# Performance work log

Hardware: AMD Instinct MI355X
Metric: run time of the kernel (lower is better)

Reference implementation:

```python
import jax, jax.numpy as jnp
import numpy as np

N = 50000   # nodes
E = 800000  # directed edges (built as reverse pairs so rev mapping is exact)
F = 64      # node_feat_dim
FE = 64     # edge_feat_dim
M = 64      # message_dim
S = 3       # num_status
L = 4       # number_layers

def _lin(key, din, dout):
    w = jax.random.normal(key, (din, dout), jnp.float32) * np.float32(1.0 / np.sqrt(din))
    return w, jnp.zeros((dout,), jnp.float32)

def setup_inputs() -> dict:
    key = jax.random.key(0)
    ks = jax.random.split(key, 16)
    half = E // 2
    s = jax.random.randint(ks[0], (half,), 0, N)
    t = jax.random.randint(ks[1], (half,), 0, N)
    src = jnp.concatenate([s, t])                      # source node of each edge
    tgt = jnp.concatenate([t, s])                      # target node of each edge
    rev = jnp.concatenate([jnp.arange(half, E), jnp.arange(half)])  # reverse-edge index
    inp = dict(src=src, tgt=tgt, rev=rev)
    inp['edge_feat_raw'] = jax.random.uniform(ks[2], (E, 1), jnp.float32)
    inp['node_prob'] = jax.random.uniform(ks[3], (N, 1), jnp.float32)
    inp['node_seed'] = (jax.random.uniform(ks[4], (N, 1)) < 0.05).astype(jnp.float32)
    inp['W_node'], inp['b_node'] = _lin(ks[5], 2, F)
    inp['W_edge'], inp['b_edge'] = _lin(ks[6], 1, FE)
    inp['W_init'], inp['b_init'] = _lin(ks[7], F + FE, M)
    inp['W_aggr'], inp['b_aggr'] = _lin(ks[8], M, M)
    inp['W_out'], inp['b_out'] = _lin(ks[9], M + F, S)
    inp['W_me'], inp['b_me'] = _lin(ks[10], FE + M, M)
    inp['W_mp'], inp['b_mp'] = _lin(ks[11], M, M)
    inp['W_ih'] = jax.random.normal(ks[12], (3 * M, M), jnp.float32) * np.float32(1.0 / np.sqrt(M))
    inp['W_hh'] = jax.random.normal(ks[13], (3 * M, M), jnp.float32) * np.float32(1.0 / np.sqrt(M))
    inp['b_ih'] = jnp.zeros((3 * M,), jnp.float32)
    inp['b_hh'] = jnp.zeros((3 * M,), jnp.float32)
    return inp

def reference(src, tgt, rev, edge_feat_raw, node_prob, node_seed,
              W_node, b_node, W_edge, b_edge, W_init, b_init,
              W_aggr, b_aggr, W_out, b_out, W_me, b_me, W_mp, b_mp,
              W_ih, W_hh, b_ih, b_hh):
    relu = jax.nn.relu
    node_feat = relu(jnp.concatenate([node_prob, node_seed], 1) @ W_node + b_node)  # [N,F]
    snode_feat = node_feat[src]                                                      # snode2edge gather [E,F]
    edge_feat = relu(edge_feat_raw @ W_edge + b_edge)                                # [E,FE]
    message = relu(jnp.concatenate([snode_feat, edge_feat], 1) @ W_init + b_init)    # [E,M]

    def nodes_out(msg):
        agg = jax.ops.segment_sum(msg, tgt, num_segments=N)                          # edge2tnode scatter-add
        agg = relu(agg @ W_aggr + b_aggr)
        logits = relu(jnp.concatenate([agg, node_feat], 1) @ W_out + b_out)
        return jax.nn.log_softmax(logits, axis=1)                                    # [N,S]

    def gru(x, h):  # torch.nn.GRUCell semantics
        gi = x @ W_ih.T + b_ih
        gh = h @ W_hh.T + b_hh
        ir, iz, in_ = jnp.split(gi, 3, axis=1)
        hr, hz, hn = jnp.split(gh, 3, axis=1)
        r = jax.nn.sigmoid(ir + hr)
        z = jax.nn.sigmoid(iz + hz)
        n = jnp.tanh(in_ + r * hn)
        return (1.0 - z) * n + z * h

    marg = [nodes_out(message)]
    deltas = []
    for _ in range(L):
        m = relu(jnp.concatenate([message, edge_feat], 1) @ W_me + b_me)
        node_agg = jax.ops.segment_sum(m, tgt, num_segments=N)
        m = node_agg[src] - m[rev]                                                   # nb_matrix (non-backtracking) spmm
        m = relu(m @ W_mp + b_mp)
        message = gru(m, message)
        marg.append(nodes_out(message))
        deltas.append(jnp.max(jnp.abs(jnp.exp(marg[-2][:, -1]) - jnp.exp(marg[-1][:, -1]))))
    return jnp.stack(marg, 0), jnp.stack(deltas)
```

## Files before the change

kernel.cpp:

```cpp
#include <hip/hip_runtime.h>
#include <hip/hip_fp16.h>

typedef _Float16 half8 __attribute__((ext_vector_type(8)));
typedef float floatx4 __attribute__((ext_vector_type(4)));

#define DEV static __device__ __forceinline__

DEV float sigmoidf_(float x) { return 1.f / (1.f + __expf(-x)); }
DEV float tanh_fast(float x) {
    x = fminf(fmaxf(x, -15.f), 15.f);
    float e2 = __expf(2.f * x);
    return (e2 - 1.f) / (e2 + 1.f);
}
DEV unsigned short f2h_(float f) {
    __half h = __float2half_rn(f);
    return *reinterpret_cast<unsigned short*>(&h);
}
DEV float h2f_(unsigned short u) {
    __half h = *reinterpret_cast<__half*>(&u);
    return __half2float(h);
}
DEV float loadElem(const float* p) { return *p; }
DEV float loadElem(const unsigned short* p) { return h2f_(*p); }
DEV void storeMsg(float* p, float v) { *p = v; }
DEV void storeMsg(unsigned short* p, float v) { *p = f2h_(v); }

DEV half8 afrag(const float* __restrict__ p, unsigned off) {
    float4 a = *reinterpret_cast<const float4*>(p + off);
    float4 b = *reinterpret_cast<const float4*>(p + off + 4);
    half8 h;
    h[0] = (_Float16)a.x; h[1] = (_Float16)a.y; h[2] = (_Float16)a.z; h[3] = (_Float16)a.w;
    h[4] = (_Float16)b.x; h[5] = (_Float16)b.y; h[6] = (_Float16)b.z; h[7] = (_Float16)b.w;
    return h;
}
DEV half8 afrag(const unsigned short* __restrict__ p, unsigned off) {
    uint4 v = *reinterpret_cast<const uint4*>(p + off);
    return __builtin_bit_cast(half8, v);
}
DEV half8 h8load(const _Float16* __restrict__ p) {
    return *reinterpret_cast<const half8*>(p);
}
DEV half8 effrag(float er, const float* __restrict__ We,
                 const float* __restrict__ be, int k0) {
    float4 w0 = *reinterpret_cast<const float4*>(We + k0);
    float4 w1 = *reinterpret_cast<const float4*>(We + k0 + 4);
    float4 b0 = *reinterpret_cast<const float4*>(be + k0);
    float4 b1 = *reinterpret_cast<const float4*>(be + k0 + 4);
    half8 h;
    h[0] = (_Float16)fmaxf(fmaf(er, w0.x, b0.x), 0.f);
    h[1] = (_Float16)fmaxf(fmaf(er, w0.y, b0.y), 0.f);
    h[2] = (_Float16)fmaxf(fmaf(er, w0.z, b0.z), 0.f);
    h[3] = (_Float16)fmaxf(fmaf(er, w0.w, b0.w), 0.f);
    h[4] = (_Float16)fmaxf(fmaf(er, w1.x, b1.x), 0.f);
    h[5] = (_Float16)fmaxf(fmaf(er, w1.y, b1.y), 0.f);
    h[6] = (_Float16)fmaxf(fmaf(er, w1.z, b1.z), 0.f);
    h[7] = (_Float16)fmaxf(fmaf(er, w1.w, b1.w), 0.f);
    return h;
}
DEV void load8(const float* __restrict__ p, float x[8]) {
    const float4* q = reinterpret_cast<const float4*>(p);
    float4 a = q[0], b = q[1];
    x[0] = a.x; x[1] = a.y; x[2] = a.z; x[3] = a.w;
    x[4] = b.x; x[5] = b.y; x[6] = b.z; x[7] = b.w;
}

__global__ void k_deg(const int* __restrict__ tgt, int* __restrict__ deg, int E) {
    int e = blockIdx.x * blockDim.x + threadIdx.x;
    if (e < E) atomicAdd(&deg[tgt[e]], 1);
}

__global__ __launch_bounds__(1024)
void k_scan(const int* __restrict__ deg, int* __restrict__ row_ptr,
            int* __restrict__ cursor, int N) {
    __shared__ int part[1024];
    int tid = threadIdx.x;
    int chunk = (N + 1023) / 1024;
    int lo = tid * chunk, hi = min(lo + chunk, N);
    int s = 0;
    for (int i = lo; i < hi; i++) s += deg[i];
    part[tid] = s;
    __syncthreads();
    for (int off = 1; off < 1024; off <<= 1) {
        int v = (tid >= off) ? part[tid - off] : 0;
        __syncthreads();
        part[tid] += v;
        __syncthreads();
    }
    int base = (tid == 0) ? 0 : part[tid - 1];
    for (int i = lo; i < hi; i++) {
        row_ptr[i] = base;
        cursor[i] = base;
        base += deg[i];
    }
    if (tid == 1023) row_ptr[N] = part[1023];
}

__global__ void k_fill(const int* __restrict__ tgt, int* __restrict__ cursor,
                       int* __restrict__ col_idx, int E) {
    int e = blockIdx.x * blockDim.x + threadIdx.x;
    if (e < E) {
        int pos = atomicAdd(&cursor[tgt[e]], 1);
        col_idx[pos] = e;
    }
}

__global__ void k_prep(const float* __restrict__ Wme, const float* __restrict__ Wmp,
                       const float* __restrict__ Wi, const float* __restrict__ Wih,
                       const float* __restrict__ Whh, _Float16* __restrict__ wp) {
    int t = blockIdx.x * blockDim.x + threadIdx.x;
    if (t < 8192) { int n = t >> 7, k = t & 127; wp[t] = (_Float16)Wme[k * 64 + n]; return; }
    int u = t - 8192;
    if (u < 4096) { int n = u >> 6, k = u & 63; wp[8192 + u] = (_Float16)Wmp[k * 64 + n]; return; }
    u -= 4096;
    if (u < 4096) { int n = u >> 6, k = u & 63; wp[12288 + u] = (_Float16)Wi[(64 + k) * 64 + n]; return; }
    u -= 4096;
    if (u < 12288) { wp[16384 + u] = (_Float16)Wih[u]; return; }
    u -= 12288;
    if (u < 12288) { wp[28672 + u] = (_Float16)Whh[u]; return; }
}

__global__ __launch_bounds__(256)
void k_zn(const float* __restrict__ prob, const float* __restrict__ seedp,
          const float* __restrict__ Wn, const float* __restrict__ bn,
          const float* __restrict__ Wi, const float* __restrict__ bi,
          float* __restrict__ zn, int N) {
    int n = blockIdx.x * blockDim.x + threadIdx.x;
    if (n >= N) return;
    float p = prob[n], sd = seedp[n];
    float acc[64];
#pragma unroll
    for (int j = 0; j < 64; j++) acc[j] = bi[j];
#pragma unroll 1
    for (int k = 0; k < 64; k++) {
        float nf = fmaxf(fmaf(p, Wn[k], fmaf(sd, Wn[64 + k], bn[k])), 0.f);
        const float* w = Wi + k * 64;
#pragma unroll
        for (int j = 0; j < 64; j++) acc[j] = fmaf(nf, w[j], acc[j]);
    }
    float4* q = reinterpret_cast<float4*>(zn + (size_t)n * 64);
#pragma unroll
    for (int c = 0; c < 16; c++)
        q[c] = make_float4(acc[4 * c], acc[4 * c + 1], acc[4 * c + 2], acc[4 * c + 3]);
}

template <typename MsgT, bool FULL>
__global__ __launch_bounds__(256)
void k_init_mfma(const int* __restrict__ src, const float* __restrict__ eraw,
                 const float* __restrict__ We, const float* __restrict__ be,
                 const _Float16* __restrict__ WibT, const float* __restrict__ zn,
                 MsgT* __restrict__ message, int row_off, int E) {
    int wid = (blockIdx.x * blockDim.x + threadIdx.x) >> 6;
    int rowbase = row_off + wid * 64;
    if (rowbase >= E) return;
    int lane = threadIdx.x & 63, q = lane >> 4, m16 = lane & 15, kq8 = q * 8;
    floatx4 zero4 = {0.f, 0.f, 0.f, 0.f};
    floatx4 acc[4][4];
#pragma unroll
    for (int a = 0; a < 4; a++)
#pragma unroll
        for (int b = 0; b < 4; b++) acc[a][b] = zero4;
#pragma unroll
    for (int ks = 0; ks < 2; ks++) {
        int k0 = ks * 32 + kq8;
        half8 B[4];
#pragma unroll
        for (int nt = 0; nt < 4; nt++) B[nt] = h8load(WibT + (nt * 16 + m16) * 64 + k0);
#pragma unroll
        for (int rt = 0; rt < 4; rt++) {
            int row = rowbase + rt * 16 + m16;
            if (!FULL) row = min(row, E - 1);
            half8 A = effrag(eraw[row], We, be, k0);
#pragma unroll
            for (int nt = 0; nt < 4; nt++)
                acc[rt][nt] = __builtin_amdgcn_mfma_f32_16x16x32_f16(A, B[nt], acc[rt][nt], 0, 0, 0);
        }
    }
#pragma unroll
    for (int nt = 0; nt < 4; nt++) {
        int col = nt * 16 + m16;
#pragma unroll
        for (int rt = 0; rt < 4; rt++)
#pragma unroll
            for (int r = 0; r < 4; r++) {
                int row = rowbase + rt * 16 + q * 4 + r;
                if (FULL || row < E) {
                    int s = src[row];
                    float v = acc[rt][nt][r] + zn[(unsigned)s * 64u + col];
                    storeMsg(message + (unsigned)row * 64u + col, fmaxf(v, 0.f));
                }
            }
    }
}

template <typename MsgT, bool FULL>
__global__ __launch_bounds__(256)
void k_edge_m_mfma(const float* __restrict__ eraw, const float* __restrict__ We,
                   const float* __restrict__ be, const _Float16* __restrict__ WmeT,
                   const float* __restrict__ bme, const MsgT* __restrict__ message,
                   unsigned short* __restrict__ m_buf, int row_off, int E) {
    int wid = (blockIdx.x * blockDim.x + threadIdx.x) >> 6;
    int rowbase = row_off + wid * 64;
    if (rowbase >= E) return;
    int lane = threadIdx.x & 63, q = lane >> 4, m16 = lane & 15, kq8 = q * 8;
    floatx4 zero4 = {0.f, 0.f, 0.f, 0.f};
    floatx4 acc[4][4];
#pragma unroll
    for (int a = 0; a < 4; a++)
#pragma unroll
        for (int b = 0; b < 4; b++) acc[a][b] = zero4;
#pragma unroll
    for (int ks = 0; ks < 4; ks++) {
        int k0 = ks * 32 + kq8;
        half8 B[4];
#pragma unroll
        for (int nt = 0; nt < 4; nt++) B[nt] = h8load(WmeT + (nt * 16 + m16) * 128 + k0);
#pragma unroll
        for (int rt = 0; rt < 4; rt++) {
            int row = rowbase + rt * 16 + m16;
            if (!FULL) row = min(row, E - 1);
            half8 A = (ks < 2) ? afrag(message + (unsigned)row * 64u, k0)
                               : effrag(eraw[row], We, be, k0 - 64);
#pragma unroll
            for (int nt = 0; nt < 4; nt++)
                acc[rt][nt] = __builtin_amdgcn_mfma_f32_16x16x32_f16(A, B[nt], acc[rt][nt], 0, 0, 0);
        }
    }
#pragma unroll
    for (int nt = 0; nt < 4; nt++) {
        int col = nt * 16 + m16;
        float bb = bme[col];
#pragma unroll
        for (int rt = 0; rt < 4; rt++)
#pragma unroll
            for (int r = 0; r < 4; r++) {
                int row = rowbase + rt * 16 + q * 4 + r;
                if (FULL || row < E)
                    m_buf[(unsigned)row * 64u + col] = f2h_(fmaxf(acc[rt][nt][r] + bb, 0.f));
            }
    }
}

template <typename MsgT, bool FULL>
__global__ __launch_bounds__(256)
void k_gru_mfma(const int* __restrict__ src, const int* __restrict__ rev,
                const float* __restrict__ node_agg,
                const unsigned short* __restrict__ m_buf,
                const _Float16* __restrict__ WmpT, const float* __restrict__ bmp,
                const _Float16* __restrict__ WihP, const _Float16* __restrict__ WhhP,
                const float* __restrict__ bih, const float* __restrict__ bhh,
                MsgT* __restrict__ message, int row_off, int E) {
    __shared__ _Float16 uT[4][64 * 72];
    int wid = (blockIdx.x * blockDim.x + threadIdx.x) >> 6;
    int rowbase = row_off + wid * 64;
    if (rowbase >= E) return;
    int w = threadIdx.x >> 6;
    int lane = threadIdx.x & 63, q = lane >> 4, m16 = lane & 15, kq8 = q * 8;
    floatx4 zero4 = {0.f, 0.f, 0.f, 0.f};

    floatx4 accU[4][4];
#pragma unroll
    for (int a = 0; a < 4; a++)
#pragma unroll
        for (int b = 0; b < 4; b++) accU[a][b] = zero4;
#pragma unroll
    for (int ks = 0; ks < 2; ks++) {
        int k0 = ks * 32 + kq8;
        half8 B[4];
#pragma unroll
        for (int nt = 0; nt < 4; nt++) B[nt] = h8load(WmpT + (nt * 16 + m16) * 64 + k0);
#pragma unroll
        for (int rt = 0; rt < 4; rt++) {
            int row = rowbase + rt * 16 + m16;
            if (!FULL) row = min(row, E - 1);
            int s = src[row], rv = rev[row];
            const float* na = node_agg + (unsigned)s * 64u + k0;
            float4 a0 = *reinterpret_cast<const float4*>(na);
            float4 a1 = *reinterpret_cast<const float4*>(na + 4);
            uint4 mv = *reinterpret_cast<const uint4*>(m_buf + (unsigned)rv * 64u + k0);
            half8 mh = __builtin_bit_cast(half8, mv);
            half8 A;
            A[0] = (_Float16)(a0.x - (float)mh[0]); A[1] = (_Float16)(a0.y - (float)mh[1]);
            A[2] = (_Float16)(a0.z - (float)mh[2]); A[3] = (_Float16)(a0.w - (float)mh[3]);
            A[4] = (_Float16)(a1.x - (float)mh[4]); A[5] = (_Float16)(a1.y - (float)mh[5]);
            A[6] = (_Float16)(a1.z - (float)mh[6]); A[7] = (_Float16)(a1.w - (float)mh[7]);
#pragma unroll
            for (int nt = 0; nt < 4; nt++)
                accU[rt][nt] = __builtin_amdgcn_mfma_f32_16x16x32_f16(A, B[nt], accU[rt][nt], 0, 0, 0);
        }
    }
#pragma unroll
    for (int nt = 0; nt < 4; nt++) {
        int col = nt * 16 + m16;
        float bb = bmp[col];
#pragma unroll
        for (int rt = 0; rt < 4; rt++)
#pragma unroll
            for (int r = 0; r < 4; r++) {
                int rl = rt * 16 + q * 4 + r;
                uT[w][rl * 72 + col] = (_Float16)fmaxf(accU[rt][nt][r] + bb, 0.f);
            }
    }
    half8 au[4][2], ah[4][2];
#pragma unroll
    for (int rt = 0; rt < 4; rt++)
#pragma unroll
        for (int ks = 0; ks < 2; ks++) {
            au[rt][ks] = *reinterpret_cast<const half8*>(
                &uT[w][(rt * 16 + m16) * 72 + ks * 32 + kq8]);
            int row = rowbase + rt * 16 + m16;
            if (!FULL) row = min(row, E - 1);
            ah[rt][ks] = afrag(message + (unsigned)row * 64u, ks * 32 + kq8);
        }
#pragma unroll 1
    for (int nt = 0; nt < 4; nt++) {
        int col = nt * 16 + m16;
        half8 Bir[2], Biz[2], Bin[2], Bhr[2], Bhz[2], Bhn[2];
#pragma unroll
        for (int ks = 0; ks < 2; ks++) {
            int k0 = ks * 32 + kq8;
            Bir[ks] = h8load(WihP + (unsigned)(0 + col) * 64u + k0);
            Biz[ks] = h8load(WihP + (unsigned)(64 + col) * 64u + k0);
            Bin[ks] = h8load(WihP + (unsigned)(128 + col) * 64u + k0);
            Bhr[ks] = h8load(WhhP + (unsigned)(0 + col) * 64u + k0);
            Bhz[ks] = h8load(WhhP + (unsigned)(64 + col) * 64u + k0);
            Bhn[ks] = h8load(WhhP + (unsigned)(128 + col) * 64u + k0);
        }
        floatx4 ar[4], az[4], ain[4], ahn[4];
#pragma unroll
        for (int rt = 0; rt < 4; rt++) { ar[rt] = zero4; az[rt] = zero4; ain[rt] = zero4; ahn[rt] = zero4; }
#pragma unroll
        for (int ks = 0; ks < 2; ks++)
#pragma unroll
            for (int rt = 0; rt < 4; rt++) {
                ar[rt] = __builtin_amdgcn_mfma_f32_16x16x32_f16(au[rt][ks], Bir[ks], ar[rt], 0, 0, 0);
                ar[rt] = __builtin_amdgcn_mfma_f32_16x16x32_f16(ah[rt][ks], Bhr[ks], ar[rt], 0, 0, 0);
                az[rt] = __builtin_amdgcn_mfma_f32_16x16x32_f16(au[rt][ks], Biz[ks], az[rt], 0, 0, 0);
                az[rt] = __builtin_amdgcn_mfma_f32_16x16x32_f16(ah[rt][ks], Bhz[ks], az[rt], 0, 0, 0);
                ain[rt] = __builtin_amdgcn_mfma_f32_16x16x32_f16(au[rt][ks], Bin[ks], ain[rt], 0, 0, 0);
                ahn[rt] = __builtin_amdgcn_mfma_f32_16x16x32_f16(ah[rt][ks], Bhn[ks], ahn[rt], 0, 0, 0);
            }
        float br_ = bih[col] + bhh[col];
        float bz_ = bih[64 + col] + bhh[64 + col];
        float bin_ = bih[128 + col];
        float bhn_ = bhh[128 + col];
#pragma unroll
        for (int rt = 0; rt < 4; rt++)
#pragma unroll
            for (int r = 0; r < 4; r++) {
                int row = rowbase + rt * 16 + q * 4 + r;
                if (FULL || row < E) {
                    float rr = sigmoidf_(ar[rt][r] + br_);
                    float zz = sigmoidf_(az[rt][r] + bz_);
                    float nn = tanh_fast(ain[rt][r] + bin_ + rr * (ahn[rt][r] + bhn_));
                    MsgT* mp = message + (unsigned)row * 64u + col;
                    float hv = loadElem(mp);
                    storeMsg(mp, fmaf(zz, hv - nn, nn));
                }
            }
    }
}

template <typename T>
__global__ __launch_bounds__(256)
void k_agg(const int* __restrict__ row_ptr, const int* __restrict__ col_idx,
           const T* __restrict__ rows, float* __restrict__ out, int N) {
    int wid = (blockIdx.x * blockDim.x + threadIdx.x) >> 6;
    int lane = threadIdx.x & 63;
    if (wid >= N) return;
    int beg = row_ptr[wid], end = row_ptr[wid + 1];
    float acc = 0.f;
    int i = beg;
    for (; i + 3 < end; i += 4) {
        int e0 = __builtin_amdgcn_readfirstlane(col_idx[i]);
        int e1 = __builtin_amdgcn_readfirstlane(col_idx[i + 1]);
        int e2 = __builtin_amdgcn_readfirstlane(col_idx[i + 2]);
        int e3 = __builtin_amdgcn_readfirstlane(col_idx[i + 3]);
        acc += loadElem(rows + (unsigned)e0 * 64u + lane);
        acc += loadElem(rows + (unsigned)e1 * 64u + lane);
        acc += loadElem(rows + (unsigned)e2 * 64u + lane);
        acc += loadElem(rows + (unsigned)e3 * 64u + lane);
    }
    for (; i < end; i++) {
        int e0 = __builtin_amdgcn_readfirstlane(col_idx[i]);
        acc += loadElem(rows + (unsigned)e0 * 64u + lane);
    }
    out[(unsigned)wid * 64u + lane] = acc;
}

__global__ __launch_bounds__(256, 2)
void k_nodes(const float* __restrict__ node_agg, const float* __restrict__ prob,
             const float* __restrict__ seedp,
             const float* __restrict__ Wn, const float* __restrict__ bn,
             const float* __restrict__ Wa, const float* __restrict__ ba,
             const float* __restrict__ Wo, const float* __restrict__ bo,
             float* __restrict__ marg, float* __restrict__ prev_p2,
             float* __restrict__ deltas_f, int layer, int N) {
    int n = blockIdx.x * blockDim.x + threadIdx.x;
    if (n >= N) return;
    float a[64];
#pragma unroll
    for (int j = 0; j < 64; j++) a[j] = ba[j];
    const float* ag = node_agg + (size_t)n * 64;
#pragma unroll 1
    for (int c = 0; c < 8; c++) {
        float v[8];
        load8(ag + 8 * c, v);
#pragma unroll
        for (int i = 0; i < 8; i++) {
            const float* w = Wa + (8 * c + i) * 64;
#pragma unroll
            for (int j = 0; j < 64; j++) a[j] = fmaf(v[i], w[j], a[j]);
        }
    }
    float l0 = bo[0], l1 = bo[1], l2 = bo[2];
#pragma unroll
    for (int k = 0; k < 64; k++) {
        float ak = fmaxf(a[k], 0.f);
        l0 = fmaf(ak, Wo[k * 3 + 0], l0);
        l1 = fmaf(ak, Wo[k * 3 + 1], l1);
        l2 = fmaf(ak, Wo[k * 3 + 2], l2);
    }
    float p = prob[n], sd = seedp[n];
#pragma unroll 1
    for (int k = 0; k < 64; k++) {
        float nf = fmaxf(fmaf(p, Wn[k], fmaf(sd, Wn[64 + k], bn[k])), 0.f);
        l0 = fmaf(nf, Wo[(64 + k) * 3 + 0], l0);
        l1 = fmaf(nf, Wo[(64 + k) * 3 + 1], l1);
        l2 = fmaf(nf, Wo[(64 + k) * 3 + 2], l2);
    }
    l0 = fmaxf(l0, 0.f); l1 = fmaxf(l1, 0.f); l2 = fmaxf(l2, 0.f);
    float mx = fmaxf(l0, fmaxf(l1, l2));
    float ssum = __expf(l0 - mx) + __expf(l1 - mx) + __expf(l2 - mx);
    float lse = mx + logf(ssum);
    float o0 = l0 - lse, o1 = l1 - lse, o2 = l2 - lse;
    float* out = marg + ((size_t)layer * N + n) * 3;
    out[0] = o0; out[1] = o1; out[2] = o2;
    float p2 = __expf(o2);
    if (layer > 0) {
        float d = fabsf(p2 - prev_p2[n]);
        atomicMax(reinterpret_cast<unsigned int*>(deltas_f + (layer - 1)),
                  __float_as_uint(d));
    }
    prev_p2[n] = p2;
}

__global__ void k_deltas_out(const float* __restrict__ deltas_f,
                             float* __restrict__ out, int L) {
    int i = threadIdx.x;
    if (i < L) out[i] = deltas_f[i];
}

template <typename MsgT>
static void run_pipeline(void* const* d_in, int E, int N, MsgT* message,
                         unsigned short* m_buf, float* node_agg, _Float16* wp,
                         int* deg, int* row_ptr, int* cursor, int* col_idx,
                         float* prev_p2, float* deltas_f, float* marg,
                         float* deltas_out, hipStream_t stream) {
    const int* src = (const int*)d_in[0];
    const int* tgt = (const int*)d_in[1];
    const int* rev = (const int*)d_in[2];
    const float* eraw = (const float*)d_in[3];
    const float* prob = (const float*)d_in[4];
    const float* seedp = (const float*)d_in[5];
    const float* Wn = (const float*)d_in[6];  const float* bn = (const float*)d_in[7];
    const float* We = (const float*)d_in[8];  const float* be = (const float*)d_in[9];
    const float* Wi = (const float*)d_in[10]; const float* bi = (const float*)d_in[11];
    const float* Wa = (const float*)d_in[12]; const float* ba = (const float*)d_in[13];
    const float* Wo = (const float*)d_in[14]; const float* bo = (const float*)d_in[15];
    const float* Wme = (const float*)d_in[16]; const float* bme = (const float*)d_in[17];
    const float* Wmp = (const float*)d_in[18]; const float* bmp = (const float*)d_in[19];
    const float* Wih = (const float*)d_in[20]; const float* Whh = (const float*)d_in[21];
    const float* bih = (const float*)d_in[22]; const float* bhh = (const float*)d_in[23];

    const _Float16* WmeT = wp;
    const _Float16* WmpT = wp + 8192;
    const _Float16* WibT = wp + 12288;
    const _Float16* WihP = wp + 16384;
    const _Float16* WhhP = wp + 28672;

    const int L = 4;
    dim3 blk(256);
    dim3 eg((E + 255) / 256), ng((N + 255) / 256);
    dim3 ag((N + 3) / 4);
    int fullb = E / 256;
    int tail_off = fullb * 256;
    bool tail = (tail_off < E);

    hipMemsetAsync(deg, 0, (size_t)N * 4, stream);
    hipMemsetAsync(deltas_f, 0, L * sizeof(float), stream);
    k_deg<<<eg, blk, 0, stream>>>(tgt, deg, E);
    k_scan<<<1, 1024, 0, stream>>>(deg, row_ptr, cursor, N);
    k_fill<<<eg, blk, 0, stream>>>(tgt, cursor, col_idx, E);
    k_prep<<<160, 256, 0, stream>>>(Wme, Wmp, Wi, Wih, Whh, wp);
    k_zn<<<ng, blk, 0, stream>>>(prob, seedp, Wn, bn, Wi, bi, node_agg, N);

    if (fullb)
        k_init_mfma<MsgT, true><<<fullb, blk, 0, stream>>>(src, eraw, We, be, WibT,
                                                           node_agg, message, 0, E);
    if (tail)
        k_init_mfma<MsgT, false><<<1, blk, 0, stream>>>(src, eraw, We, be, WibT,
                                                        node_agg, message, tail_off, E);
    k_agg<MsgT><<<ag, blk, 0, stream>>>(row_ptr, col_idx, message, node_agg, N);
    k_nodes<<<ng, blk, 0, stream>>>(node_agg, prob, seedp, Wn, bn, Wa, ba, Wo, bo,
                                    marg, prev_p2, deltas_f, 0, N);
    for (int l = 0; l < L; l++) {
        if (fullb)
            k_edge_m_mfma<MsgT, true><<<fullb, blk, 0, stream>>>(eraw, We, be, WmeT, bme,
                                                                 message, m_buf, 0, E);
        if (tail)
            k_edge_m_mfma<MsgT, false><<<1, blk, 0, stream>>>(eraw, We, be, WmeT, bme,
                                                              message, m_buf, tail_off, E);
        k_agg<unsigned short><<<ag, blk, 0, stream>>>(row_ptr, col_idx, m_buf,
                                                      node_agg, N);
        if (fullb)
            k_gru_mfma<MsgT, true><<<fullb, blk, 0, stream>>>(src, rev, node_agg, m_buf,
                                                              WmpT, bmp, WihP, WhhP,
                                                              bih, bhh, message, 0, E);
        if (tail)
            k_gru_mfma<MsgT, false><<<1, blk, 0, stream>>>(src, rev, node_agg, m_buf,
                                                           WmpT, bmp, WihP, WhhP,
                                                           bih, bhh, message, tail_off, E);
        k_agg<MsgT><<<ag, blk, 0, stream>>>(row_ptr, col_idx, message, node_agg, N);
        k_nodes<<<ng, blk, 0, stream>>>(node_agg, prob, seedp, Wn, bn, Wa, ba,
                                        Wo, bo, marg, prev_p2, deltas_f, l + 1, N);
    }
    k_deltas_out<<<1, 64, 0, stream>>>(deltas_f, deltas_out, L);
}

extern "C" void kernel_launch(void* const* d_in, const int* in_sizes, int n_in,
                              void* d_out, int out_size, void* d_ws, size_t ws_size,
                              hipStream_t stream) {
    const int E = in_sizes[0];
    const int N = in_sizes[4];
    const int L = 4, S = 3;

    float* marg = (float*)d_out;
    float* deltas_out = marg + (size_t)(L + 1) * N * S;

    char* ws = (char*)d_ws;
    float* deltas_f = (float*)ws;
    float* prev_p2 = (float*)(ws + 16);
    int* deg = (int*)(prev_p2 + N);
    int* row_ptr = deg + N;
    int* cursor = row_ptr + N + 1;
    int* col_idx = cursor + N;
    char* p = (char*)(col_idx + E);
    p = (char*)(((uintptr_t)p + 255) & ~(uintptr_t)255);
    _Float16* wp = (_Float16*)p;
    p += 40960 * 2;
    p = (char*)(((uintptr_t)p + 255) & ~(uintptr_t)255);
    float* node_agg = (float*)p;
    p += (size_t)N * 64 * 4;
    p = (char*)(((uintptr_t)p + 255) & ~(uintptr_t)255);
    size_t head = (size_t)(p - ws);
    size_t msg_f32 = (size_t)E * 64 * 4;
    size_t msg_f16 = (size_t)E * 64 * 2;
    size_t m_f16 = (size_t)E * 64 * 2;

    if (ws_size >= head + msg_f32 + m_f16) {
        float* message = (float*)p;
        unsigned short* m_buf = (unsigned short*)(p + msg_f32);
        run_pipeline<float>(d_in, E, N, message, m_buf, node_agg, wp,
                            deg, row_ptr, cursor, col_idx,
                            prev_p2, deltas_f, marg, deltas_out, stream);
    } else {
        unsigned short* message = (unsigned short*)p;
        unsigned short* m_buf = (unsigned short*)(p + msg_f16);
        run_pipeline<unsigned short>(d_in, E, N, message, m_buf, node_agg, wp,
                                     deg, row_ptr, cursor, col_idx,
                                     prev_p2, deltas_f, marg, deltas_out, stream);
    }
}
```

Measured before the change: 1.998 ms.

## Process 16-row subtiles sequentially in edge MFMA kernels and widen aggregation unroll

The init, edge-message and GRU MFMA kernels now walk each wave's 64 rows one 16-row subtile at a time in a non-unrolled loop, instead of holding a 4x4 accumulator grid and all A fragments at once. This shrinks accumulator and fragment register use, and the GRU's shared-memory staging buffer drops from 64 to 16 rows per wave, with the aim of raising occupancy. In exchange, weight B fragments are reloaded for every subtile rather than reused across four row tiles. The aggregation kernel is unrolled to 8 gathered rows per iteration with two accumulators, to keep more loads in flight.

New measurement: 2.659 ms. 1.33x slower.

```diff
diff --git a/kernel.cpp b/kernel.cpp
--- a/kernel.cpp
+++ b/kernel.cpp
@@ -154,41 +154,37 @@
     if (rowbase >= E) return;
     int lane = threadIdx.x & 63, q = lane >> 4, m16 = lane & 15, kq8 = q * 8;
     floatx4 zero4 = {0.f, 0.f, 0.f, 0.f};
-    floatx4 acc[4][4];
-#pragma unroll
-    for (int a = 0; a < 4; a++)
-#pragma unroll
-        for (int b = 0; b < 4; b++) acc[a][b] = zero4;
-#pragma unroll
-    for (int ks = 0; ks < 2; ks++) {
-        int k0 = ks * 32 + kq8;
-        half8 B[4];
-#pragma unroll
-        for (int nt = 0; nt < 4; nt++) B[nt] = h8load(WibT + (nt * 16 + m16) * 64 + k0);
-#pragma unroll
-        for (int rt = 0; rt < 4; rt++) {
-            int row = rowbase + rt * 16 + m16;
-            if (!FULL) row = min(row, E - 1);
-            half8 A = effrag(eraw[row], We, be, k0);
-#pragma unroll
-            for (int nt = 0; nt < 4; nt++)
-                acc[rt][nt] = __builtin_amdgcn_mfma_f32_16x16x32_f16(A, B[nt], acc[rt][nt], 0, 0, 0);
-        }
-    }
-#pragma unroll
-    for (int nt = 0; nt < 4; nt++) {
-        int col = nt * 16 + m16;
-#pragma unroll
-        for (int rt = 0; rt < 4; rt++)
+#pragma unroll 1
+    for (int rt = 0; rt < 4; rt++) {
+        int rbase = rowbase + rt * 16;
+        int row = rbase + m16;
+        if (!FULL) row = min(row, E - 1);
+        float er = eraw[row];
+        half8 A0 = effrag(er, We, be, kq8);
+        half8 A1 = effrag(er, We, be, 32 + kq8);
+        floatx4 acc[4];
+#pragma unroll
+        for (int nt = 0; nt < 4; nt++) acc[nt] = zero4;
+#pragma unroll
+        for (int nt = 0; nt < 4; nt++) {
+            half8 B0 = h8load(WibT + (nt * 16 + m16) * 64 + kq8);
+            half8 B1 = h8load(WibT + (nt * 16 + m16) * 64 + 32 + kq8);
+            acc[nt] = __builtin_amdgcn_mfma_f32_16x16x32_f16(A0, B0, acc[nt], 0, 0, 0);
+            acc[nt] = __builtin_amdgcn_mfma_f32_16x16x32_f16(A1, B1, acc[nt], 0, 0, 0);
+        }
+#pragma unroll
+        for (int nt = 0; nt < 4; nt++) {
+            int col = nt * 16 + m16;
 #pragma unroll
             for (int r = 0; r < 4; r++) {
-                int row = rowbase + rt * 16 + q * 4 + r;
-                if (FULL || row < E) {
-                    int s = src[row];
-                    float v = acc[rt][nt][r] + zn[(unsigned)s * 64u + col];
-                    storeMsg(message + (unsigned)row * 64u + col, fmaxf(v, 0.f));
+                int orow = rbase + q * 4 + r;
+                if (FULL || orow < E) {
+                    int s = src[orow];
+                    float v = acc[nt][r] + zn[(unsigned)s * 64u + col];
+                    storeMsg(message + (unsigned)orow * 64u + col, fmaxf(v, 0.f));
                 }
             }
+        }
     }
 }
 
@@ -203,40 +199,39 @@
     if (rowbase >= E) return;
     int lane = threadIdx.x & 63, q = lane >> 4, m16 = lane & 15, kq8 = q * 8;
     floatx4 zero4 = {0.f, 0.f, 0.f, 0.f};
-    floatx4 acc[4][4];
-#pragma unroll
-    for (int a = 0; a < 4; a++)
-#pragma unroll
-        for (int b = 0; b < 4; b++) acc[a][b] = zero4;
-#pragma unroll
-    for (int ks = 0; ks < 4; ks++) {
-        int k0 = ks * 32 + kq8;
-        half8 B[4];
-#pragma unroll
-        for (int nt = 0; nt < 4; nt++) B[nt] = h8load(WmeT + (nt * 16 + m16) * 128 + k0);
-#pragma unroll
-        for (int rt = 0; rt < 4; rt++) {
-            int row = rowbase + rt * 16 + m16;
-            if (!FULL) row = min(row, E - 1);
-            half8 A = (ks < 2) ? afrag(message + (unsigned)row * 64u, k0)
-                               : effrag(eraw[row], We, be, k0 - 64);
-#pragma unroll
-            for (int nt = 0; nt < 4; nt++)
-                acc[rt][nt] = __builtin_amdgcn_mfma_f32_16x16x32_f16(A, B[nt], acc[rt][nt], 0, 0, 0);
-        }
-    }
-#pragma unroll
-    for (int nt = 0; nt < 4; nt++) {
-        int col = nt * 16 + m16;
-        float bb = bme[col];
-#pragma unroll
-        for (int rt = 0; rt < 4; rt++)
+#pragma unroll 1
+    for (int rt = 0; rt < 4; rt++) {
+        int rbase = rowbase + rt * 16;
+        int row = rbase + m16;
+        if (!FULL) row = min(row, E - 1);
+        float er = eraw[row];
+        half8 A[4];
+        A[0] = afrag(message + (unsigned)row * 64u, kq8);
+        A[1] = afrag(message + (unsigned)row * 64u, 32 + kq8);
+        A[2] = effrag(er, We, be, kq8);
+        A[3] = effrag(er, We, be, 32 + kq8);
+        floatx4 acc[4];
+#pragma unroll
+        for (int nt = 0; nt < 4; nt++) acc[nt] = zero4;
+#pragma unroll
+        for (int ks = 0; ks < 4; ks++) {
+#pragma unroll
+            for (int nt = 0; nt < 4; nt++) {
+                half8 B = h8load(WmeT + (nt * 16 + m16) * 128 + ks * 32 + kq8);
+                acc[nt] = __builtin_amdgcn_mfma_f32_16x16x32_f16(A[ks], B, acc[nt], 0, 0, 0);
+            }
+        }
+#pragma unroll
+        for (int nt = 0; nt < 4; nt++) {
+            int col = nt * 16 + m16;
+            float bb = bme[col];
 #pragma unroll
             for (int r = 0; r < 4; r++) {
-                int row = rowbase + rt * 16 + q * 4 + r;
-                if (FULL || row < E)
-                    m_buf[(unsigned)row * 64u + col] = f2h_(fmaxf(acc[rt][nt][r] + bb, 0.f));
+                int orow = rbase + q * 4 + r;
+                if (FULL || orow < E)
+                    m_buf[(unsigned)orow * 64u + col] = f2h_(fmaxf(acc[nt][r] + bb, 0.f));
             }
+        }
     }
 }
 
@@ -249,7 +244,7 @@
                 const _Float16* __restrict__ WihP, const _Float16* __restrict__ WhhP,
                 const float* __restrict__ bih, const float* __restrict__ bhh,
                 MsgT* __restrict__ message, int row_off, int E) {
-    __shared__ _Float16 uT[4][64 * 72];
+    __shared__ _Float16 uT[4][16 * 72];
     int wid = (blockIdx.x * blockDim.x + threadIdx.x) >> 6;
     int rowbase = row_off + wid * 64;
     if (rowbase >= E) return;
@@ -257,22 +252,21 @@
     int lane = threadIdx.x & 63, q = lane >> 4, m16 = lane & 15, kq8 = q * 8;
     floatx4 zero4 = {0.f, 0.f, 0.f, 0.f};
 
-    floatx4 accU[4][4];
-#pragma unroll
-    for (int a = 0; a < 4; a++)
-#pragma unroll
-        for (int b = 0; b < 4; b++) accU[a][b] = zero4;
-#pragma unroll
-    for (int ks = 0; ks < 2; ks++) {
-        int k0 = ks * 32 + kq8;
-        half8 B[4];
-#pragma unroll
-        for (int nt = 0; nt < 4; nt++) B[nt] = h8load(WmpT + (nt * 16 + m16) * 64 + k0);
-#pragma unroll
-        for (int rt = 0; rt < 4; rt++) {
-            int row = rowbase + rt * 16 + m16;
-            if (!FULL) row = min(row, E - 1);
-            int s = src[row], rv = rev[row];
+#pragma unroll 1
+    for (int rt = 0; rt < 4; rt++) {
+        int rbase = rowbase + rt * 16;
+        int row = rbase + m16;
+        if (!FULL) row = min(row, E - 1);
+        int s = src[row], rv = rev[row];
+        half8 ah0 = afrag(message + (unsigned)row * 64u, kq8);
+        half8 ah1 = afrag(message + (unsigned)row * 64u, 32 + kq8);
+
+        floatx4 accU[4];
+#pragma unroll
+        for (int nt = 0; nt < 4; nt++) accU[nt] = zero4;
+#pragma unroll
+        for (int ks = 0; ks < 2; ks++) {
+            int k0 = ks * 32 + kq8;
             const float* na = node_agg + (unsigned)s * 64u + k0;
             float4 a0 = *reinterpret_cast<const float4*>(na);
             float4 a1 = *reinterpret_cast<const float4*>(na + 4);
@@ -284,79 +278,61 @@
             A[4] = (_Float16)(a1.x - (float)mh[4]); A[5] = (_Float16)(a1.y - (float)mh[5]);
             A[6] = (_Float16)(a1.z - (float)mh[6]); A[7] = (_Float16)(a1.w - (float)mh[7]);
 #pragma unroll
-            for (int nt = 0; nt < 4; nt++)
-                accU[rt][nt] = __builtin_amdgcn_mfma_f32_16x16x32_f16(A, B[nt], accU[rt][nt], 0, 0, 0);
-        }
-    }
-#pragma unroll
-    for (int nt = 0; nt < 4; nt++) {
-        int col = nt * 16 + m16;
-        float bb = bmp[col];
-#pragma unroll
-        for (int rt = 0; rt < 4; rt++)
+            for (int nt = 0; nt < 4; nt++) {
+                half8 B = h8load(WmpT + (nt * 16 + m16) * 64 + k0);
+                accU[nt] = __builtin_amdgcn_mfma_f32_16x16x32_f16(A, B, accU[nt], 0, 0, 0);
+            }
+        }
+#pragma unroll
+        for (int nt = 0; nt < 4; nt++) {
+            int col = nt * 16 + m16;
+            float bb = bmp[col];
+#pragma unroll
+            for (int r = 0; r < 4; r++)
+                uT[w][(q * 4 + r) * 72 + col] = (_Float16)fmaxf(accU[nt][r] + bb, 0.f);
+        }
+        half8 au0 = *reinterpret_cast<const half8*>(&uT[w][m16 * 72 + kq8]);
+        half8 au1 = *reinterpret_cast<const half8*>(&uT[w][m16 * 72 + 32 + kq8]);
+
+#pragma unroll 1
+        for (int nt = 0; nt < 4; nt++) {
+            int col = nt * 16 + m16;
+            floatx4 ar = zero4, az = zero4, ain = zero4, ahn = zero4;
+#pragma unroll
+            for (int ks = 0; ks < 2; ks++) {
+                int k0 = ks * 32 + kq8;
+                half8 au = ks ? au1 : au0;
+                half8 ah = ks ? ah1 : ah0;
+                half8 Bir = h8load(WihP + (unsigned)(0 + col) * 64u + k0);
+                half8 Biz = h8load(WihP + (unsigned)(64 + col) * 64u + k0);
+                half8 Bin = h8load(WihP + (unsigned)(128 + col) * 64u + k0);
+                half8 Bhr = h8load(WhhP + (unsigned)(0 + col) * 64u + k0);
+                half8 Bhz = h8load(WhhP + (unsigned)(64 + col) * 64u + k0);
+                half8 Bhn = h8load(WhhP + (unsigned)(128 + col) * 64u + k0);
+                ar = __builtin_amdgcn_mfma_f32_16x16x32_f16(au, Bir, ar, 0, 0, 0);
+                ar = __builtin_amdgcn_mfma_f32_16x16x32_f16(ah, Bhr, ar, 0, 0, 0);
+                az = __builtin_amdgcn_mfma_f32_16x16x32_f16(au, Biz, az, 0, 0, 0);
+                az = __builtin_amdgcn_mfma_f32_16x16x32_f16(ah, Bhz, az, 0, 0, 0);
+                ain = __builtin_amdgcn_mfma_f32_16x16x32_f16(au, Bin, ain, 0, 0, 0);
+                ahn = __builtin_amdgcn_mfma_f32_16x16x32_f16(ah, Bhn, ahn, 0, 0, 0);
+            }
+            float br_ = bih[col] + bhh[col];
+            float bz_ = bih[64 + col] + bhh[64 + col];
+            float bin_ = bih[128 + col];
+            float bhn_ = bhh[128 + col];
 #pragma unroll
             for (int r = 0; r < 4; r++) {
-                int rl = rt * 16 + q * 4 + r;
-                uT[w][rl * 72 + col] = (_Float16)fmaxf(accU[rt][nt][r] + bb, 0.f);
-            }
-    }
-    half8 au[4][2], ah[4][2];
-#pragma unroll
-    for (int rt = 0; rt < 4; rt++)
-#pragma unroll
-        for (int ks = 0; ks < 2; ks++) {
-            au[rt][ks] = *reinterpret_cast<const half8*>(
-                &uT[w][(rt * 16 + m16) * 72 + ks * 32 + kq8]);
-            int row = rowbase + rt * 16 + m16;
-            if (!FULL) row = min(row, E - 1);
-            ah[rt][ks] = afrag(message + (unsigned)row * 64u, ks * 32 + kq8);
-        }
-#pragma unroll 1
-    for (int nt = 0; nt < 4; nt++) {
-        int col = nt * 16 + m16;
-        half8 Bir[2], Biz[2], Bin[2], Bhr[2], Bhz[2], Bhn[2];
-#pragma unroll
-        for (int ks = 0; ks < 2; ks++) {
-            int k0 = ks * 32 + kq8;
-            Bir[ks] = h8load(WihP + (unsigned)(0 + col) * 64u + k0);
-            Biz[ks] = h8load(WihP + (unsigned)(64 + col) * 64u + k0);
-            Bin[ks] = h8load(WihP + (unsigned)(128 + col) * 64u + k0);
-            Bhr[ks] = h8load(WhhP + (unsigned)(0 + col) * 64u + k0);
-            Bhz[ks] = h8load(WhhP + (unsigned)(64 + col) * 64u + k0);
-            Bhn[ks] = h8load(WhhP + (unsigned)(128 + col) * 64u + k0);
-        }
-        floatx4 ar[4], az[4], ain[4], ahn[4];
-#pragma unroll
-        for (int rt = 0; rt < 4; rt++) { ar[rt] = zero4; az[rt] = zero4; ain[rt] = zero4; ahn[rt] = zero4; }
-#pragma unroll
-        for (int ks = 0; ks < 2; ks++)
-#pragma unroll
-            for (int rt = 0; rt < 4; rt++) {
-                ar[rt] = __builtin_amdgcn_mfma_f32_16x16x32_f16(au[rt][ks], Bir[ks], ar[rt], 0, 0, 0);
-                ar[rt] = __builtin_amdgcn_mfma_f32_16x16x32_f16(ah[rt][ks], Bhr[ks], ar[rt], 0, 0, 0);
-                az[rt] = __builtin_amdgcn_mfma_f32_16x16x32_f16(au[rt][ks], Biz[ks], az[rt], 0, 0, 0);
-                az[rt] = __builtin_amdgcn_mfma_f32_16x16x32_f16(ah[rt][ks], Bhz[ks], az[rt], 0, 0, 0);
-                ain[rt] = __builtin_amdgcn_mfma_f32_16x16x32_f16(au[rt][ks], Bin[ks], ain[rt], 0, 0, 0);
-                ahn[rt] = __builtin_amdgcn_mfma_f32_16x16x32_f16(ah[rt][ks], Bhn[ks], ahn[rt], 0, 0, 0);
-            }
-        float br_ = bih[col] + bhh[col];
-        float bz_ = bih[64 + col] + bhh[64 + col];
-        float bin_ = bih[128 + col];
-        float bhn_ = bhh[128 + col];
-#pragma unroll
-        for (int rt = 0; rt < 4; rt++)
-#pragma unroll
-            for (int r = 0; r < 4; r++) {
-                int row = rowbase + rt * 16 + q * 4 + r;
-                if (FULL || row < E) {
-                    float rr = sigmoidf_(ar[rt][r] + br_);
-                    float zz = sigmoidf_(az[rt][r] + bz_);
-                    float nn = tanh_fast(ain[rt][r] + bin_ + rr * (ahn[rt][r] + bhn_));
-                    MsgT* mp = message + (unsigned)row * 64u + col;
+                int orow = rbase + q * 4 + r;
+                if (FULL || orow < E) {
+                    float rr = sigmoidf_(ar[r] + br_);
+                    float zz = sigmoidf_(az[r] + bz_);
+                    float nn = tanh_fast(ain[r] + bin_ + rr * (ahn[r] + bhn_));
+                    MsgT* mp = message + (unsigned)orow * 64u + col;
                     float hv = loadElem(mp);
                     storeMsg(mp, fmaf(zz, hv - nn, nn));
                 }
             }
+        }
     }
 }
 
@@ -368,23 +344,31 @@
     int lane = threadIdx.x & 63;
     if (wid >= N) return;
     int beg = row_ptr[wid], end = row_ptr[wid + 1];
-    float acc = 0.f;
+    float acc = 0.f, acc2 = 0.f;
     int i = beg;
-    for (; i + 3 < end; i += 4) {
+    for (; i + 7 < end; i += 8) {
         int e0 = __builtin_amdgcn_readfirstlane(col_idx[i]);
         int e1 = __builtin_amdgcn_readfirstlane(col_idx[i + 1]);
         int e2 = __builtin_amdgcn_readfirstlane(col_idx[i + 2]);
         int e3 = __builtin_amdgcn_readfirstlane(col_idx[i + 3]);
+        int e4 = __builtin_amdgcn_readfirstlane(col_idx[i + 4]);
+        int e5 = __builtin_amdgcn_readfirstlane(col_idx[i + 5]);
+        int e6 = __builtin_amdgcn_readfirstlane(col_idx[i + 6]);
+        int e7 = __builtin_amdgcn_readfirstlane(col_idx[i + 7]);
         acc += loadElem(rows + (unsigned)e0 * 64u + lane);
-        acc += loadElem(rows + (unsigned)e1 * 64u + lane);
+        acc2 += loadElem(rows + (unsigned)e1 * 64u + lane);
         acc += loadElem(rows + (unsigned)e2 * 64u + lane);
-        acc += loadElem(rows + (unsigned)e3 * 64u + lane);
+        acc2 += loadElem(rows + (unsigned)e3 * 64u + lane);
+        acc += loadElem(rows + (unsigned)e4 * 64u + lane);
+        acc2 += loadElem(rows + (unsigned)e5 * 64u + lane);
+        acc += loadElem(rows + (unsigned)e6 * 64u + lane);
+        acc2 += loadElem(rows + (unsigned)e7 * 64u + lane);
     }
     for (; i < end; i++) {
         int e0 = __builtin_amdgcn_readfirstlane(col_idx[i]);
         acc += loadElem(rows + (unsigned)e0 * 64u + lane);
     }
-    out[(unsigned)wid * 64u + lane] = acc;
+    out[(unsigned)wid * 64u + lane] = acc + acc2;
 }
 
 __global__ __launch_bounds__(256, 2)
```
